# Optimization experiments

Measured on AMD Instinct MI355X. Metric: run time of the kernel, lower is better.

The kernel has to match this reference:

```python
import jax, jax.numpy as jnp
import numpy as np

B, NC, H, W, NT = 8, 2048, 128, 128, 4096
EPS = 1e-6


def _off_grid_interp(pts, vals, q):
    """Piecewise-linear scattered interpolation (Delaunay surrogate).
    pts: (Nc,2), vals: (Nc,1), q: (Nt,2) -> (Nt,1).
    For each query, take the 3 nearest context points, compute barycentric
    weights in that triangle; outside/degenerate falls back to mean fill,
    mirroring LinearNDInterpolator(fill_value=vals.mean()).
    """
    d2 = jnp.sum((q[:, None, :] - pts[None, :, :]) ** 2, axis=-1)  # (Nt, Nc)
    _, idx = jax.lax.top_k(-d2, 3)                                  # (Nt, 3)
    tri = pts[idx]                                                  # (Nt, 3, 2)
    tv = vals[idx]                                                  # (Nt, 3, 1)
    p0 = tri[:, 0]
    e1 = tri[:, 1] - p0
    e2 = tri[:, 2] - p0
    r = q - p0
    det = e1[:, 0] * e2[:, 1] - e1[:, 1] * e2[:, 0]
    det_safe = jnp.where(jnp.abs(det) < EPS, 1.0, det)
    w1 = (r[:, 0] * e2[:, 1] - r[:, 1] * e2[:, 0]) / det_safe
    w2 = (e1[:, 0] * r[:, 1] - e1[:, 1] * r[:, 0]) / det_safe
    w0 = 1.0 - w1 - w2
    inside = (w0 >= -EPS) & (w1 >= -EPS) & (w2 >= -EPS) & (jnp.abs(det) >= EPS)
    interp = (w0[:, None] * tv[:, 0] + w1[:, None] * tv[:, 1]
              + w2[:, None] * tv[:, 2])                             # (Nt, 1)
    fill = jnp.mean(vals)
    return jnp.where(inside[:, None], interp, fill)


def _on_grid_interp(grid_x, grid_y, vals, q):
    """Bilinear interpolation on a rectilinear grid (scipy.interpolate.interpn,
    method='linear', bounds_error=False, fill_value=vals.mean()).
    grid_x: (H,), grid_y: (W,), vals: (H,W,1), q: (Nt,2) -> (Nt,1).
    """
    qx, qy = q[:, 0], q[:, 1]
    ix = jnp.clip(jnp.searchsorted(grid_x, qx) - 1, 0, grid_x.shape[0] - 2)
    iy = jnp.clip(jnp.searchsorted(grid_y, qy) - 1, 0, grid_y.shape[0] - 2)
    tx = ((qx - grid_x[ix]) / (grid_x[ix + 1] - grid_x[ix]))[:, None]
    ty = ((qy - grid_y[iy]) / (grid_y[iy + 1] - grid_y[iy]))[:, None]
    v00 = vals[ix, iy]
    v01 = vals[ix, iy + 1]
    v10 = vals[ix + 1, iy]
    v11 = vals[ix + 1, iy + 1]
    interp = (v00 * (1 - tx) * (1 - ty) + v10 * tx * (1 - ty)
              + v01 * (1 - tx) * ty + v11 * tx * ty)
    inside = ((qx >= grid_x[0]) & (qx <= grid_x[-1])
              & (qy >= grid_y[0]) & (qy <= grid_y[-1]))
    fill = jnp.mean(vals)
    return jnp.where(inside[:, None], interp, fill)


def setup_inputs() -> dict:
    key = jax.random.key(0)
    ks = jax.random.split(key, 6)
    xc_off_grid = jax.random.uniform(ks[0], (B, NC, 2), minval=-1.0, maxval=1.0)
    yc_off_grid = jax.random.normal(ks[1], (B, NC, 1))
    gx = jnp.linspace(-1.0, 1.0, H)
    gy = jnp.linspace(-1.0, 1.0, W)
    grid = jnp.stack(jnp.meshgrid(gx, gy, indexing='ij'), axis=-1)  # (H,W,2)
    xc_on_grid = jnp.broadcast_to(grid, (B, H, W, 2))
    yc_on_grid = jax.random.normal(ks[2], (B, H, W, 1))
    xt = jax.random.uniform(ks[3], (B, NT, 2), minval=-1.0, maxval=1.0)
    mix_w = jax.random.normal(ks[4], (2, 1)) * 0.5
    mix_b = jax.random.normal(ks[5], (1,)) * 0.1
    return dict(xc_off_grid=xc_off_grid, yc_off_grid=yc_off_grid,
                xc_on_grid=xc_on_grid, yc_on_grid=yc_on_grid, xt=xt,
                mix_w=mix_w, mix_b=mix_b)


def reference(xc_off_grid, yc_off_grid, xc_on_grid, yc_on_grid, xt, mix_w, mix_b):
    # off-grid scattered interpolation, vmapped over batch
    yt_off = jax.vmap(_off_grid_interp)(xc_off_grid, yc_off_grid, xt)  # (B,Nt,1)
    # on-grid: axis coordinates exactly as the original (bxc_on[:,0,0], bxc_on[0,:,1])
    gx = xc_on_grid[:, :, 0, 0]  # (B, H)
    gy = xc_on_grid[:, 0, :, 1]  # (B, W)
    yt_on = jax.vmap(_on_grid_interp)(gx, gy, yc_on_grid, xt)          # (B,Nt,1)
    yt = jnp.concatenate([yt_off, yt_on], axis=-1)                     # (B,Nt,2)
    return yt @ mix_w + mix_b                                          # (B,Nt,1)
```

## Files before the change

### kernel.cpp

```cpp
#include <hip/hip_runtime.h>
#include <math.h>

#define NB   8
#define NC   2048
#define HH   128
#define WW   128
#define NTQ  4096
#define EPSF 1e-6f
#define CELLW 0.125f
#define BLK  512
#define QPB  128
#define LPQ  4
#define UMAX 0xFFFFFFFFFFFFFFFFULL

typedef unsigned long long u64;

__device__ __forceinline__ void ins3u(u64 u, u64& U0, u64& U1, u64& U2) {
    bool lt2 = u < U2, lt1 = u < U1, lt0 = u < U0;
    U2 = lt1 ? U1 : (lt2 ? u : U2);
    U1 = lt0 ? U0 : (lt1 ? u : U1);
    U0 = lt0 ? u  : U0;
}

__global__ __launch_bounds__(BLK) void fused_interp_kernel(
    const float* __restrict__ xc_off,
    const float* __restrict__ yc_off,
    const float* __restrict__ xc_on,
    const float* __restrict__ yc_on,
    const float* __restrict__ xt,
    const float* __restrict__ mw,
    const float* __restrict__ mb,
    float* __restrict__ out)
{
#pragma clang fp contract(off)
    __shared__ float4 spts[NC];
    __shared__ int    shist[256];
    __shared__ int    soffs[257];
    __shared__ int    scur[256];
    __shared__ float  sgx[HH];
    __shared__ float  sgy[WW];
    __shared__ float  sred[8];

    const int tid   = threadIdx.x;
    const int b     = blockIdx.x >> 5;
    const int qbase = (blockIdx.x & 31) * QPB;

    if (tid < 256) shist[tid] = 0;
    const float* xob = xc_on + (size_t)b * HH * WW * 2;
    if (tid >= 256 && tid < 256 + HH) sgx[tid - 256] = xob[(size_t)(tid - 256) * (WW * 2)];
    if (tid >= 384 && tid < 384 + WW) sgy[tid - 384] = xob[2 * (tid - 384) + 1];
    __syncthreads();

    const float2* xcb = (const float2*)(xc_off + (size_t)b * NC * 2);
    const float*  ycb = yc_off + (size_t)b * NC;
    float2 pp_[4]; float vv_[4]; int cc_[4];
    float vsum = 0.f;
#pragma unroll
    for (int t = 0; t < 4; ++t) {
        int k = tid + t * BLK;
        float2 P = xcb[k];
        float  V = ycb[k];
        pp_[t] = P; vv_[t] = V;
        int cx = (int)floorf((P.x + 1.0f) * 8.0f); cx = min(max(cx, 0), 15);
        int cy = (int)floorf((P.y + 1.0f) * 8.0f); cy = min(max(cy, 0), 15);
        cc_[t] = cy * 16 + cx;
        atomicAdd(&shist[cc_[t]], 1);
        vsum += V;
    }
    for (int o = 32; o > 0; o >>= 1) vsum += __shfl_down(vsum, o);
    if ((tid & 63) == 0) sred[tid >> 6] = vsum;
    __syncthreads();

    if (tid < 64) {
        int h0 = shist[4*tid], h1 = shist[4*tid+1], h2 = shist[4*tid+2], h3 = shist[4*tid+3];
        int s = h0 + h1 + h2 + h3; int tot = s;
        for (int off = 1; off < 64; off <<= 1) {
            int u = __shfl_up(s, off);
            if (tid >= off) s += u;
        }
        int excl = s - tot;
        soffs[4*tid]   = excl;
        soffs[4*tid+1] = excl + h0;
        soffs[4*tid+2] = excl + h0 + h1;
        soffs[4*tid+3] = excl + h0 + h1 + h2;
        if (tid == 63) soffs[256] = excl + tot;
    }
    __syncthreads();
    if (tid < 256) scur[tid] = soffs[tid];
    __syncthreads();

#pragma unroll
    for (int t = 0; t < 4; ++t) {
        int k = tid + t * BLK;
        int pos = atomicAdd(&scur[cc_[t]], 1);
        float4 o4; o4.x = pp_[t].x; o4.y = pp_[t].y; o4.z = vv_[t]; o4.w = __int_as_float(k);
        spts[pos] = o4;
    }
    __syncthreads();

    const float fillv = (sred[0] + sred[1] + sred[2] + sred[3] +
                         sred[4] + sred[5] + sred[6] + sred[7]) / (float)NC;

    const int g   = tid & (LPQ - 1);
    const int grp = tid >> 2;
    const int q   = qbase + grp;
    const float qx = xt[((size_t)b * NTQ + q) * 2];
    const float qy = xt[((size_t)b * NTQ + q) * 2 + 1];
    int qcx = (int)floorf((qx + 1.0f) * 8.0f); qcx = min(max(qcx, 0), 15);
    int qcy = (int)floorf((qy + 1.0f) * 8.0f); qcy = min(max(qcy, 0), 15);

    u64 P0 = UMAX, P1 = UMAX, P2 = UMAX;
    u64 F0 = UMAX, F1 = UMAX, F2 = UMAX;

    for (int row = 0; row < 3; ++row) {
        int cy = qcy + row - 1;
        if (cy < 0 || cy > 15) continue;
        int c0 = cy * 16 + max(qcx - 1, 0);
        int c1 = cy * 16 + min(qcx + 1, 15);
        int s = soffs[c0], e = soffs[c1 + 1];
        for (int k = s + g; k < e; k += LPQ) {
            float4 P = spts[k];
            float dx = qx - P.x, dy = qy - P.y;
            float dd = dx * dx + dy * dy;
            u64 u = ((u64)__float_as_uint(dd) << 32) | (unsigned int)__float_as_int(P.w);
            ins3u(u, F0, F1, F2);
        }
    }
    for (int m = 1; m <= 2; m <<= 1) {
        u64 e0 = __shfl_xor(F0, m), e1 = __shfl_xor(F1, m), e2 = __shfl_xor(F2, m);
        ins3u(e0, F0, F1, F2);
        ins3u(e1, F0, F1, F2);
        ins3u(e2, F0, F1, F2);
    }
    P0 = F0; P1 = F1; P2 = F2;

    float bnd = 1.0f * CELLW - 1e-6f;
    u64 thr = ((u64)__float_as_uint(bnd * bnd)) << 32;
    bool done = P2 < thr;

    for (int r = 2; r <= 15; ++r) {
        if (__all(done)) break;
        if (!done) {
            F0 = F1 = F2 = UMAX;
            for (int t = g; t < 8 * r; t += LPQ) {
                int side = t / (2 * r), u = t % (2 * r);
                int dx, dy;
                if (side == 0)      { dx = -r + u; dy = -r; }
                else if (side == 1) { dx = r;      dy = -r + u; }
                else if (side == 2) { dx = r - u;  dy = r; }
                else                { dx = -r;     dy = r - u; }
                int cx = qcx + dx, cy = qcy + dy;
                if (cx < 0 || cx > 15 || cy < 0 || cy > 15) continue;
                int c = cy * 16 + cx;
                int s = soffs[c], e = soffs[c + 1];
                for (int k = s; k < e; ++k) {
                    float4 P = spts[k];
                    float ddx = qx - P.x, ddy = qy - P.y;
                    float dd = ddx * ddx + ddy * ddy;
                    u64 uu = ((u64)__float_as_uint(dd) << 32) | (unsigned int)__float_as_int(P.w);
                    ins3u(uu, F0, F1, F2);
                }
            }
            for (int m = 1; m <= 2; m <<= 1) {
                u64 e0 = __shfl_xor(F0, m), e1 = __shfl_xor(F1, m), e2 = __shfl_xor(F2, m);
                ins3u(e0, F0, F1, F2);
                ins3u(e1, F0, F1, F2);
                ins3u(e2, F0, F1, F2);
            }
            ins3u(F0, P0, P1, P2);
            ins3u(F1, P0, P1, P2);
            ins3u(F2, P0, P1, P2);
            float bb = (float)r * CELLW - 1e-6f;
            u64 tt = ((u64)__float_as_uint(bb * bb)) << 32;
            done = P2 < tt;
        }
    }

    if (g == 0) {
        int J0 = (int)(P0 & 0xFFFFFFFFULL);
        int J1 = (int)(P1 & 0xFFFFFFFFULL);
        int J2 = (int)(P2 & 0xFFFFFFFFULL);
        float2 A  = xcb[J0];
        float2 Bp = xcb[J1];
        float2 C  = xcb[J2];
        float e1x = Bp.x - A.x, e1y = Bp.y - A.y;
        float e2x = C.x  - A.x, e2y = C.y  - A.y;
        float rx  = qx - A.x,   ry  = qy - A.y;
        float det = e1x * e2y - e1y * e2x;
        float adet = fabsf(det);
        float dets = (adet < EPSF) ? 1.0f : det;
        float w1 = (rx * e2y - ry * e2x) / dets;
        float w2 = (e1x * ry - e1y * rx) / dets;
        float w0 = 1.0f - w1 - w2;
        bool inside = (w0 >= -EPSF) && (w1 >= -EPSF) && (w2 >= -EPSF) && (adet >= EPSF);
        float interp = w0 * ycb[J0] + w1 * ycb[J1] + w2 * ycb[J2];
        float yoff = inside ? interp : fillv;

        int ix = (int)((qx + 1.0f) * 63.5f);
        ix = min(max(ix, 0), HH - 2);
        while (ix > 0 && !(sgx[ix] < qx)) --ix;
        while (ix < HH - 2 && sgx[ix + 1] < qx) ++ix;
        int iy = (int)((qy + 1.0f) * 63.5f);
        iy = min(max(iy, 0), WW - 2);
        while (iy > 0 && !(sgy[iy] < qy)) --iy;
        while (iy < WW - 2 && sgy[iy + 1] < qy) ++iy;

        float x0 = sgx[ix], x1 = sgx[ix + 1];
        float y0 = sgy[iy], y1 = sgy[iy + 1];
        float tx = (qx - x0) / (x1 - x0);
        float ty = (qy - y0) / (y1 - y0);
        const float* yob = yc_on + (size_t)b * HH * WW;
        float v00 = yob[ix * WW + iy];
        float v01 = yob[ix * WW + iy + 1];
        float v10 = yob[(ix + 1) * WW + iy];
        float v11 = yob[(ix + 1) * WW + iy + 1];
        float yon = v00 * (1.f - tx) * (1.f - ty)
                  + v10 * tx * (1.f - ty)
                  + v01 * (1.f - tx) * ty
                  + v11 * tx * ty;

        out[(size_t)b * NTQ + q] = yoff * mw[0] + yon * mw[1] + mb[0];
    }
}

extern "C" void kernel_launch(void* const* d_in, const int* in_sizes, int n_in,
                              void* d_out, int out_size, void* d_ws, size_t ws_size,
                              hipStream_t stream) {
    const float* xc_off = (const float*)d_in[0];
    const float* yc_off = (const float*)d_in[1];
    const float* xc_on  = (const float*)d_in[2];
    const float* yc_on  = (const float*)d_in[3];
    const float* xt     = (const float*)d_in[4];
    const float* mix_w  = (const float*)d_in[5];
    const float* mix_b  = (const float*)d_in[6];
    float* out = (float*)d_out;

    fused_interp_kernel<<<NB * (NTQ / QPB), BLK, 0, stream>>>(
        xc_off, yc_off, xc_on, yc_on, xt, mix_w, mix_b, out);
}
```

Baseline: 12.78 us.

## Use 8 lanes per query, halve queries per block, compact epilogue via shared memory

Each query is now searched by 8 lanes instead of 4, with 64 queries per block, so the grid doubles to 512 blocks. After the neighbour search, winning indices go to shared memory so that 64 contiguous threads run the barycentric and bilinear epilogue, instead of one lane in every group of 4. Query coordinates are now read as float2. The cost is that each block rebuilds the per-batch spatial binning of all 2048 context points, and there are twice as many blocks, so that setup is repeated twice as often, plus an extra barrier and a longer shuffle reduction.

```diff
diff --git a/kernel.cpp b/kernel.cpp
--- a/kernel.cpp
+++ b/kernel.cpp
@@ -9,8 +9,8 @@
 #define EPSF 1e-6f
 #define CELLW 0.125f
 #define BLK  512
-#define QPB  128
-#define LPQ  4
+#define QPB  64
+#define LPQ  8
 #define UMAX 0xFFFFFFFFFFFFFFFFULL
 
 typedef unsigned long long u64;
@@ -40,10 +40,11 @@
     __shared__ float  sgx[HH];
     __shared__ float  sgy[WW];
     __shared__ float  sred[8];
+    __shared__ int4   sres[QPB];
 
     const int tid   = threadIdx.x;
-    const int b     = blockIdx.x >> 5;
-    const int qbase = (blockIdx.x & 31) * QPB;
+    const int b     = blockIdx.x >> 6;
+    const int qbase = (blockIdx.x & 63) * QPB;
 
     if (tid < 256) shist[tid] = 0;
     const float* xob = xc_on + (size_t)b * HH * WW * 2;
@@ -102,10 +103,10 @@
                          sred[4] + sred[5] + sred[6] + sred[7]) / (float)NC;
 
     const int g   = tid & (LPQ - 1);
-    const int grp = tid >> 2;
+    const int grp = tid >> 3;
     const int q   = qbase + grp;
-    const float qx = xt[((size_t)b * NTQ + q) * 2];
-    const float qy = xt[((size_t)b * NTQ + q) * 2 + 1];
+    const float2 Q = ((const float2*)xt)[(size_t)b * NTQ + q];
+    const float qx = Q.x, qy = Q.y;
     int qcx = (int)floorf((qx + 1.0f) * 8.0f); qcx = min(max(qcx, 0), 15);
     int qcy = (int)floorf((qy + 1.0f) * 8.0f); qcy = min(max(qcy, 0), 15);
 
@@ -126,7 +127,7 @@
             ins3u(u, F0, F1, F2);
         }
     }
-    for (int m = 1; m <= 2; m <<= 1) {
+    for (int m = 1; m <= 4; m <<= 1) {
         u64 e0 = __shfl_xor(F0, m), e1 = __shfl_xor(F1, m), e2 = __shfl_xor(F2, m);
         ins3u(e0, F0, F1, F2);
         ins3u(e1, F0, F1, F2);
@@ -161,7 +162,7 @@
                     ins3u(uu, F0, F1, F2);
                 }
             }
-            for (int m = 1; m <= 2; m <<= 1) {
+            for (int m = 1; m <= 4; m <<= 1) {
                 u64 e0 = __shfl_xor(F0, m), e1 = __shfl_xor(F1, m), e2 = __shfl_xor(F2, m);
                 ins3u(e0, F0, F1, F2);
                 ins3u(e1, F0, F1, F2);
@@ -177,15 +178,27 @@
     }
 
     if (g == 0) {
-        int J0 = (int)(P0 & 0xFFFFFFFFULL);
-        int J1 = (int)(P1 & 0xFFFFFFFFULL);
-        int J2 = (int)(P2 & 0xFFFFFFFFULL);
+        int4 r4;
+        r4.x = (int)(P0 & 0xFFFFFFFFULL);
+        r4.y = (int)(P1 & 0xFFFFFFFFULL);
+        r4.z = (int)(P2 & 0xFFFFFFFFULL);
+        r4.w = 0;
+        sres[grp] = r4;
+    }
+    __syncthreads();
+
+    if (tid < QPB) {
+        const int4 r4 = sres[tid];
+        const int J0 = r4.x, J1 = r4.y, J2 = r4.z;
+        const float2 Qe = ((const float2*)xt)[(size_t)b * NTQ + qbase + tid];
+        const float ex = Qe.x, ey = Qe.y;
+
         float2 A  = xcb[J0];
         float2 Bp = xcb[J1];
         float2 C  = xcb[J2];
         float e1x = Bp.x - A.x, e1y = Bp.y - A.y;
         float e2x = C.x  - A.x, e2y = C.y  - A.y;
-        float rx  = qx - A.x,   ry  = qy - A.y;
+        float rx  = ex - A.x,   ry  = ey - A.y;
         float det = e1x * e2y - e1y * e2x;
         float adet = fabsf(det);
         float dets = (adet < EPSF) ? 1.0f : det;
@@ -196,19 +209,19 @@
         float interp = w0 * ycb[J0] + w1 * ycb[J1] + w2 * ycb[J2];
         float yoff = inside ? interp : fillv;
 
-        int ix = (int)((qx + 1.0f) * 63.5f);
+        int ix = (int)((ex + 1.0f) * 63.5f);
         ix = min(max(ix, 0), HH - 2);
-        while (ix > 0 && !(sgx[ix] < qx)) --ix;
-        while (ix < HH - 2 && sgx[ix + 1] < qx) ++ix;
-        int iy = (int)((qy + 1.0f) * 63.5f);
+        while (ix > 0 && !(sgx[ix] < ex)) --ix;
+        while (ix < HH - 2 && sgx[ix + 1] < ex) ++ix;
+        int iy = (int)((ey + 1.0f) * 63.5f);
         iy = min(max(iy, 0), WW - 2);
-        while (iy > 0 && !(sgy[iy] < qy)) --iy;
-        while (iy < WW - 2 && sgy[iy + 1] < qy) ++iy;
+        while (iy > 0 && !(sgy[iy] < ey)) --iy;
+        while (iy < WW - 2 && sgy[iy + 1] < ey) ++iy;
 
         float x0 = sgx[ix], x1 = sgx[ix + 1];
         float y0 = sgy[iy], y1 = sgy[iy + 1];
-        float tx = (qx - x0) / (x1 - x0);
-        float ty = (qy - y0) / (y1 - y0);
+        float tx = (ex - x0) / (x1 - x0);
+        float ty = (ey - y0) / (y1 - y0);
         const float* yob = yc_on + (size_t)b * HH * WW;
         float v00 = yob[ix * WW + iy];
         float v01 = yob[ix * WW + iy + 1];
@@ -219,7 +232,7 @@
                   + v01 * (1.f - tx) * ty
                   + v11 * tx * ty;
 
-        out[(size_t)b * NTQ + q] = yoff * mw[0] + yon * mw[1] + mb[0];
+        out[(size_t)b * NTQ + qbase + tid] = yoff * mw[0] + yon * mw[1] + mb[0];
     }
 }
 
```

New measurement: 13.73 us. 7.4% more time.

## Replace counting-sort grid with fixed-capacity cell buckets and use 8 lanes per query

Applied to the files above, without the earlier changes.

The prefix-scan counting sort (histogram, scan, scatter, several block barriers) is replaced by fixed-capacity per-cell buckets filled in one atomic pass, with a small global spill list for overflowing cells. The 3x3 neighbourhood scan becomes a fully unrolled predicated loop over slots, and lanes per query rise from 4 to 8 with half as many queries per block. Block indices now interleave batches. This cuts setup barriers and scatter work, but doubles the number of blocks that each rebuild the point grid, and overflow beyond the spill capacity would drop points.

```diff
diff --git a/kernel.cpp b/kernel.cpp
--- a/kernel.cpp
+++ b/kernel.cpp
@@ -9,8 +9,10 @@
 #define EPSF 1e-6f
 #define CELLW 0.125f
 #define BLK  512
-#define QPB  128
-#define LPQ  4
+#define QPB  64
+#define LPQ  8
+#define CAP  16
+#define SPCAP 256
 #define UMAX 0xFFFFFFFFFFFFFFFFULL
 
 typedef unsigned long long u64;
@@ -22,7 +24,7 @@
     U0 = lt0 ? u  : U0;
 }
 
-__global__ __launch_bounds__(BLK) void fused_interp_kernel(
+__global__ __launch_bounds__(BLK, 4) void fused_interp_kernel(
     const float* __restrict__ xc_off,
     const float* __restrict__ yc_off,
     const float* __restrict__ xc_on,
@@ -33,19 +35,23 @@
     float* __restrict__ out)
 {
 #pragma clang fp contract(off)
-    __shared__ float4 spts[NC];
-    __shared__ int    shist[256];
-    __shared__ int    soffs[257];
-    __shared__ int    scur[256];
+    __shared__ float2 sxy[256 * CAP];
+    __shared__ int    sidx[256 * CAP];
+    __shared__ int    scnt[256];
+    __shared__ float2 spxy[SPCAP];
+    __shared__ int    spidx[SPCAP];
+    __shared__ int    sspill;
     __shared__ float  sgx[HH];
     __shared__ float  sgy[WW];
     __shared__ float  sred[8];
 
     const int tid   = threadIdx.x;
-    const int b     = blockIdx.x >> 5;
-    const int qbase = (blockIdx.x & 31) * QPB;
-
-    if (tid < 256) shist[tid] = 0;
+    const int bid   = blockIdx.x;
+    const int b     = bid & 7;
+    const int qbase = (bid >> 3) * QPB;
+
+    if (tid < 256) scnt[tid] = 0;
+    if (tid == 0) sspill = 0;
     const float* xob = xc_on + (size_t)b * HH * WW * 2;
     if (tid >= 256 && tid < 256 + HH) sgx[tid - 256] = xob[(size_t)(tid - 256) * (WW * 2)];
     if (tid >= 384 && tid < 384 + WW) sgy[tid - 384] = xob[2 * (tid - 384) + 1];
@@ -53,80 +59,76 @@
 
     const float2* xcb = (const float2*)(xc_off + (size_t)b * NC * 2);
     const float*  ycb = yc_off + (size_t)b * NC;
-    float2 pp_[4]; float vv_[4]; int cc_[4];
     float vsum = 0.f;
 #pragma unroll
     for (int t = 0; t < 4; ++t) {
         int k = tid + t * BLK;
         float2 P = xcb[k];
-        float  V = ycb[k];
-        pp_[t] = P; vv_[t] = V;
-        int cx = (int)floorf((P.x + 1.0f) * 8.0f); cx = min(max(cx, 0), 15);
-        int cy = (int)floorf((P.y + 1.0f) * 8.0f); cy = min(max(cy, 0), 15);
-        cc_[t] = cy * 16 + cx;
-        atomicAdd(&shist[cc_[t]], 1);
-        vsum += V;
+        vsum += ycb[k];
+        int cx = min(max((int)floorf((P.x + 1.0f) * 8.0f), 0), 15);
+        int cy = min(max((int)floorf((P.y + 1.0f) * 8.0f), 0), 15);
+        int c = cy * 16 + cx;
+        int slot = atomicAdd(&scnt[c], 1);
+        if (slot < CAP) {
+            sxy[c * CAP + slot] = P;
+            sidx[c * CAP + slot] = k;
+        } else {
+            int sp = atomicAdd(&sspill, 1);
+            if (sp < SPCAP) { spxy[sp] = P; spidx[sp] = k; }
+        }
     }
     for (int o = 32; o > 0; o >>= 1) vsum += __shfl_down(vsum, o);
     if ((tid & 63) == 0) sred[tid >> 6] = vsum;
     __syncthreads();
 
-    if (tid < 64) {
-        int h0 = shist[4*tid], h1 = shist[4*tid+1], h2 = shist[4*tid+2], h3 = shist[4*tid+3];
-        int s = h0 + h1 + h2 + h3; int tot = s;
-        for (int off = 1; off < 64; off <<= 1) {
-            int u = __shfl_up(s, off);
-            if (tid >= off) s += u;
-        }
-        int excl = s - tot;
-        soffs[4*tid]   = excl;
-        soffs[4*tid+1] = excl + h0;
-        soffs[4*tid+2] = excl + h0 + h1;
-        soffs[4*tid+3] = excl + h0 + h1 + h2;
-        if (tid == 63) soffs[256] = excl + tot;
-    }
-    __syncthreads();
-    if (tid < 256) scur[tid] = soffs[tid];
-    __syncthreads();
-
-#pragma unroll
-    for (int t = 0; t < 4; ++t) {
-        int k = tid + t * BLK;
-        int pos = atomicAdd(&scur[cc_[t]], 1);
-        float4 o4; o4.x = pp_[t].x; o4.y = pp_[t].y; o4.z = vv_[t]; o4.w = __int_as_float(k);
-        spts[pos] = o4;
-    }
-    __syncthreads();
-
-    const float fillv = (sred[0] + sred[1] + sred[2] + sred[3] +
-                         sred[4] + sred[5] + sred[6] + sred[7]) / (float)NC;
-
     const int g   = tid & (LPQ - 1);
-    const int grp = tid >> 2;
+    const int grp = tid >> 3;
     const int q   = qbase + grp;
-    const float qx = xt[((size_t)b * NTQ + q) * 2];
-    const float qy = xt[((size_t)b * NTQ + q) * 2 + 1];
-    int qcx = (int)floorf((qx + 1.0f) * 8.0f); qcx = min(max(qcx, 0), 15);
-    int qcy = (int)floorf((qy + 1.0f) * 8.0f); qcy = min(max(qcy, 0), 15);
+    const float2 Q = ((const float2*)xt)[(size_t)b * NTQ + q];
+    const float qx = Q.x, qy = Q.y;
+    const int qcx = min(max((int)floorf((qx + 1.0f) * 8.0f), 0), 15);
+    const int qcy = min(max((int)floorf((qy + 1.0f) * 8.0f), 0), 15);
+
+    int cbase[9], ccnt[9];
+#pragma unroll
+    for (int i = 0; i < 9; ++i) {
+        int cx = qcx + (i % 3) - 1, cy = qcy + (i / 3) - 1;
+        bool ok = (cx >= 0) && (cx <= 15) && (cy >= 0) && (cy <= 15);
+        int c = ok ? (cy * 16 + cx) : 0;
+        cbase[i] = c * CAP;
+        ccnt[i]  = ok ? min(scnt[c], CAP) : 0;
+    }
 
     u64 P0 = UMAX, P1 = UMAX, P2 = UMAX;
     u64 F0 = UMAX, F1 = UMAX, F2 = UMAX;
 
-    for (int row = 0; row < 3; ++row) {
-        int cy = qcy + row - 1;
-        if (cy < 0 || cy > 15) continue;
-        int c0 = cy * 16 + max(qcx - 1, 0);
-        int c1 = cy * 16 + min(qcx + 1, 15);
-        int s = soffs[c0], e = soffs[c1 + 1];
-        for (int k = s + g; k < e; k += LPQ) {
-            float4 P = spts[k];
+#pragma unroll
+    for (int i = 0; i < 9; ++i) {
+#pragma unroll
+        for (int h = 0; h < 2; ++h) {
+            int slot = g + 8 * h;
+            bool valid = slot < ccnt[i];
+            int a = cbase[i] + slot;
+            float2 P = sxy[a];
+            int   id = sidx[a];
             float dx = qx - P.x, dy = qy - P.y;
             float dd = dx * dx + dy * dy;
-            u64 u = ((u64)__float_as_uint(dd) << 32) | (unsigned int)__float_as_int(P.w);
+            u64 u = valid ? (((u64)__float_as_uint(dd) << 32) | (unsigned int)id) : UMAX;
             ins3u(u, F0, F1, F2);
         }
     }
-    for (int m = 1; m <= 2; m <<= 1) {
+    {
+        int ns = min(sspill, SPCAP);
+        for (int k = g; k < ns; k += LPQ) {
+            float2 P = spxy[k];
+            int   id = spidx[k];
+            float dx = qx - P.x, dy = qy - P.y;
+            float dd = dx * dx + dy * dy;
+            u64 u = ((u64)__float_as_uint(dd) << 32) | (unsigned int)id;
+            ins3u(u, F0, F1, F2);
+        }
+    }
+    for (int m = 1; m <= 4; m <<= 1) {
         u64 e0 = __shfl_xor(F0, m), e1 = __shfl_xor(F1, m), e2 = __shfl_xor(F2, m);
         ins3u(e0, F0, F1, F2);
         ins3u(e1, F0, F1, F2);
@@ -152,16 +154,17 @@
                 int cx = qcx + dx, cy = qcy + dy;
                 if (cx < 0 || cx > 15 || cy < 0 || cy > 15) continue;
                 int c = cy * 16 + cx;
-                int s = soffs[c], e = soffs[c + 1];
-                for (int k = s; k < e; ++k) {
-                    float4 P = spts[k];
+                int cnt = min(scnt[c], CAP);
+                for (int s = 0; s < cnt; ++s) {
+                    float2 P = sxy[c * CAP + s];
+                    int   id = sidx[c * CAP + s];
                     float ddx = qx - P.x, ddy = qy - P.y;
                     float dd = ddx * ddx + ddy * ddy;
-                    u64 uu = ((u64)__float_as_uint(dd) << 32) | (unsigned int)__float_as_int(P.w);
+                    u64 uu = ((u64)__float_as_uint(dd) << 32) | (unsigned int)id;
                     ins3u(uu, F0, F1, F2);
                 }
             }
-            for (int m = 1; m <= 2; m <<= 1) {
+            for (int m = 1; m <= 4; m <<= 1) {
                 u64 e0 = __shfl_xor(F0, m), e1 = __shfl_xor(F1, m), e2 = __shfl_xor(F2, m);
                 ins3u(e0, F0, F1, F2);
                 ins3u(e1, F0, F1, F2);
@@ -177,9 +180,12 @@
     }
 
     if (g == 0) {
-        int J0 = (int)(P0 & 0xFFFFFFFFULL);
-        int J1 = (int)(P1 & 0xFFFFFFFFULL);
-        int J2 = (int)(P2 & 0xFFFFFFFFULL);
+        const float fillv = (sred[0] + sred[1] + sred[2] + sred[3] +
+                             sred[4] + sred[5] + sred[6] + sred[7]) / (float)NC;
+        const int J0 = (int)(P0 & 0xFFFFFFFFULL);
+        const int J1 = (int)(P1 & 0xFFFFFFFFULL);
+        const int J2 = (int)(P2 & 0xFFFFFFFFULL);
+
         float2 A  = xcb[J0];
         float2 Bp = xcb[J1];
         float2 C  = xcb[J2];
```

Result: slower. 16.45 us (+28.7%).
